# Kernel optimization log

Hardware: AMD Instinct MI355X
Metric: run time of the kernel (lower is better)

## Reference

```python
import jax, jax.numpy as jnp
import numpy as np

N = 100000      # nodes
E = 1600000     # edges
IN_FEATS = 256
HID = 64
N_LAYERS = 3
OUT_FEATS = 32


def _glorot(key, shape):
    lim = np.sqrt(6.0 / (shape[0] + shape[1]))
    return jax.random.uniform(key, shape, jnp.float32, -lim, lim)


def setup_inputs() -> dict:
    key = jax.random.key(0)
    ks = jax.random.split(key, 8)
    feat = jax.random.normal(ks[0], (N, IN_FEATS), jnp.float32)
    src = jax.random.randint(ks[1], (E,), 0, N, jnp.int32)
    dst = jax.random.randint(ks[2], (E,), 0, N, jnp.int32)
    W1 = _glorot(ks[3], (IN_FEATS, HID)); b1 = jnp.zeros((HID,), jnp.float32)
    W2 = _glorot(ks[4], (HID, HID));      b2 = jnp.zeros((HID,), jnp.float32)
    W3 = _glorot(ks[5], (HID, HID));      b3 = jnp.zeros((HID,), jnp.float32)
    Wm = _glorot(ks[6], (HID * N_LAYERS, OUT_FEATS))
    bm = jnp.zeros((OUT_FEATS,), jnp.float32)
    return dict(feat=feat, src=src, dst=dst, W1=W1, b1=b1, W2=W2, b2=b2,
                W3=W3, b3=b3, Wm=Wm, bm=bm)


def _gcn_layer(feat, W, b, src, dst, do_isqrt, di_isqrt):
    # DGL GraphConv, norm='both', eval-mode dropout (identity), ReLU activation.
    # Weight applied before aggregation (mathematically identical, smaller SpMM).
    h = (feat * do_isqrt[:, None]) @ W            # [N, hid]
    agg = jax.ops.segment_sum(h[src], dst, num_segments=N)  # copy_u / sum
    return jax.nn.relu(agg * di_isqrt[:, None] + b)


def reference(feat, src, dst, W1, b1, W2, b2, W3, b3, Wm, bm):
    ones = jnp.ones((E,), jnp.float32)
    deg_out = jnp.clip(jax.ops.segment_sum(ones, src, num_segments=N), 1.0)
    deg_in = jnp.clip(jax.ops.segment_sum(ones, dst, num_segments=N), 1.0)
    do_isqrt = deg_out ** -0.5
    di_isqrt = deg_in ** -0.5

    h1 = _gcn_layer(feat, W1, b1, src, dst, do_isqrt, di_isqrt)
    h2 = _gcn_layer(h1, W2, b2, src, dst, do_isqrt, di_isqrt)
    h3 = _gcn_layer(h2, W3, b3, src, dst, do_isqrt, di_isqrt)

    # Jumping knowledge: mode='cat'
    h = jnp.concatenate([h1, h2, h3], axis=-1)    # [N, 192]
    # Final un-normalized message pass: copy_u / sum
    h = jax.ops.segment_sum(h[src], dst, num_segments=N)
    return h @ Wm + bm                            # [N, 32]
```

## Files before the change

### kernel.cpp

```cpp
#include <hip/hip_runtime.h>
#include <hip/hip_fp8.h>

#define IN_FEATS 256
#define HID 64
#define OUTF 32
#define JK (3*HID)

#define NB    128
#define BSH   10
#define NBLK2 256

typedef __attribute__((ext_vector_type(4))) float floatx4;
typedef __attribute__((ext_vector_type(8))) short shortx8;

__device__ inline unsigned short f2bf(float f) {
    unsigned u = __float_as_uint(f);
    unsigned r = (u + 0x7fffu + ((u >> 16) & 1u)) >> 16;
    return (unsigned short)r;
}
__device__ inline float bf2f(unsigned short u) {
    return __uint_as_float(((unsigned)u) << 16);
}
__device__ inline unsigned pack2(float a, float b) {
    return (unsigned)f2bf(a) | ((unsigned)f2bf(b) << 16);
}
__device__ inline unsigned char f2q(float f) {
    __hip_fp8_e4m3 q(f);
    return (unsigned char)q.__x;
}
__device__ inline float q2f(unsigned char b) {
    union { unsigned char c; __hip_fp8_e4m3 q; } u;
    u.c = b;
    return (float)u.q;
}
__device__ inline void accq8(uint2 u, float* a, float s) {
    a[0] = fmaf(q2f((unsigned char)(u.x      )), s, a[0]);
    a[1] = fmaf(q2f((unsigned char)(u.x >>  8)), s, a[1]);
    a[2] = fmaf(q2f((unsigned char)(u.x >> 16)), s, a[2]);
    a[3] = fmaf(q2f((unsigned char)(u.x >> 24)), s, a[3]);
    a[4] = fmaf(q2f((unsigned char)(u.y      )), s, a[4]);
    a[5] = fmaf(q2f((unsigned char)(u.y >>  8)), s, a[5]);
    a[6] = fmaf(q2f((unsigned char)(u.y >> 16)), s, a[6]);
    a[7] = fmaf(q2f((unsigned char)(u.y >> 24)), s, a[7]);
}
__device__ inline void acc8(uint4 u, float* a) {
    a[0] += bf2f((unsigned short)(u.x & 0xffff)); a[1] += bf2f((unsigned short)(u.x >> 16));
    a[2] += bf2f((unsigned short)(u.y & 0xffff)); a[3] += bf2f((unsigned short)(u.y >> 16));
    a[4] += bf2f((unsigned short)(u.z & 0xffff)); a[5] += bf2f((unsigned short)(u.z >> 16));
    a[6] += bf2f((unsigned short)(u.w & 0xffff)); a[7] += bf2f((unsigned short)(u.w >> 16));
}

__device__ inline void chunk_bounds(int E, int b, int& beg, int& end) {
    int cb = ((E + NBLK2 - 1) / NBLK2 + 3) & ~3;
    beg = b * cb;
    end = min(beg + cb, E);
}

__global__ __launch_bounds__(256) void p1_hist(const int* __restrict__ src,
                                               const int* __restrict__ dst, int E,
                                               int* __restrict__ bhd, int* __restrict__ bhs) {
    __shared__ int hd[NB], hs[NB];
    int b = blockIdx.x;
    for (int t = threadIdx.x; t < NB; t += 256) { hd[t] = 0; hs[t] = 0; }
    __syncthreads();
    int beg, end;
    chunk_bounds(E, b, beg, end);
    int e = beg + threadIdx.x * 4;
    for (; e + 4 <= end; e += 1024) {
        int4 dd = *(const int4*)&dst[e];
        int4 ss = *(const int4*)&src[e];
        atomicAdd(&hd[dd.x >> BSH], 1); atomicAdd(&hd[dd.y >> BSH], 1);
        atomicAdd(&hd[dd.z >> BSH], 1); atomicAdd(&hd[dd.w >> BSH], 1);
        atomicAdd(&hs[ss.x >> BSH], 1); atomicAdd(&hs[ss.y >> BSH], 1);
        atomicAdd(&hs[ss.z >> BSH], 1); atomicAdd(&hs[ss.w >> BSH], 1);
    }
    for (; e < end; ++e) {
        atomicAdd(&hd[dst[e] >> BSH], 1);
        atomicAdd(&hs[src[e] >> BSH], 1);
    }
    __syncthreads();
    for (int t = threadIdx.x; t < NB; t += 256) {
        bhd[b * NB + t] = hd[t];
        bhs[b * NB + t] = hs[t];
    }
}

__global__ __launch_bounds__(256) void p2a_tot(const int* __restrict__ bhd,
                                               const int* __restrict__ bhs,
                                               int* __restrict__ totd, int* __restrict__ tots,
                                               int nblk,
                                               const float* __restrict__ W1, const float* __restrict__ W2,
                                               const float* __restrict__ W3, const float* __restrict__ Wm,
                                               unsigned short* __restrict__ W1t, unsigned short* __restrict__ W2t,
                                               unsigned short* __restrict__ W3t, unsigned short* __restrict__ Wmt) {
    if ((int)blockIdx.x >= 2 * NB) {
        int i = (blockIdx.x - 2 * NB) * 256 + threadIdx.x;
        if (i < 256 * 64) { int k = i / 64, c = i % 64; W1t[c * 256 + k] = f2bf(W1[i]); return; }
        int j = i - 256 * 64;
        if (j < 64 * 64) { int k = j / 64, c = j % 64; W2t[c * 64 + k] = f2bf(W2[j]); return; }
        int j2 = j - 64 * 64;
        if (j2 < 64 * 64) { int k = j2 / 64, c = j2 % 64; W3t[c * 64 + k] = f2bf(W3[j2]); return; }
        int j3 = j2 - 64 * 64;
        if (j3 < 192 * 32) { int k = j3 / 32, c = j3 % 32; Wmt[c * 192 + k] = f2bf(Wm[j3]); }
        return;
    }
    __shared__ int s[256];
    int side = blockIdx.x >> 7;
    int t = blockIdx.x & (NB - 1);
    const int* bh = side ? bhs : bhd;
    int acc = 0;
    for (int k = threadIdx.x; k < nblk; k += 256) acc += bh[k * NB + t];
    s[threadIdx.x] = acc;
    __syncthreads();
    for (int off = 128; off > 0; off >>= 1) {
        if (threadIdx.x < off) s[threadIdx.x] += s[threadIdx.x + off];
        __syncthreads();
    }
    if (threadIdx.x == 0) (side ? tots : totd)[t] = s[0];
}

__global__ __launch_bounds__(128) void p2b_scan(const int* __restrict__ totd,
                                                const int* __restrict__ tots,
                                                int* __restrict__ based, int* __restrict__ bases) {
    __shared__ int s[NB];
    const int* tot = blockIdx.x ? tots : totd;
    int* bb = blockIdx.x ? bases : based;
    int t = threadIdx.x;
    int v = tot[t];
    s[t] = v;
    __syncthreads();
    for (int off = 1; off < NB; off <<= 1) {
        int u = (t >= off) ? s[t - off] : 0;
        __syncthreads();
        s[t] += u;
        __syncthreads();
    }
    bb[t] = s[t] - v;
    if (t == NB - 1) bb[NB] = s[NB - 1];
}

__global__ __launch_bounds__(256) void p2c_off(int* __restrict__ bhd, int* __restrict__ bhs,
                                               const int* __restrict__ based,
                                               const int* __restrict__ bases, int nblk) {
    __shared__ int s[256];
    int side = blockIdx.x >> 7;
    int t = blockIdx.x & (NB - 1);
    int* bh = side ? bhs : bhd;
    int carry = (side ? bases : based)[t];
    for (int k0 = 0; k0 < nblk; k0 += 256) {
        int k = k0 + threadIdx.x;
        int v = (k < nblk) ? bh[k * NB + t] : 0;
        s[threadIdx.x] = v;
        __syncthreads();
        for (int off = 1; off < 256; off <<= 1) {
            int u = (threadIdx.x >= off) ? s[threadIdx.x - off] : 0;
            __syncthreads();
            s[threadIdx.x] += u;
            __syncthreads();
        }
        if (k < nblk) bh[k * NB + t] = carry + s[threadIdx.x] - v;
        int tot = s[255];
        __syncthreads();
        carry += tot;
    }
}

__global__ __launch_bounds__(256) void p3m(
    const int* __restrict__ src, const int* __restrict__ dst, int E,
    const int* __restrict__ bhd, const int* __restrict__ bhs,
    int* __restrict__ pairbuf, int* __restrict__ srctmp,
    const float* __restrict__ feat, const unsigned short* __restrict__ W1t,
    unsigned char* __restrict__ outq, int nrows) {
    __shared__ int curd[NB], curs[NB];
    __shared__ unsigned short Al[64 * 64];
    __shared__ unsigned short Bl[64 * 64];

    if ((int)blockIdx.x < NBLK2) {
        int b = blockIdx.x;
        for (int t = threadIdx.x; t < NB; t += 256) {
            curd[t] = bhd[b * NB + t];
            curs[t] = bhs[b * NB + t];
        }
        __syncthreads();
        int beg, end;
        chunk_bounds(E, b, beg, end);
        int e = beg + threadIdx.x * 4;
        for (; e + 4 <= end; e += 1024) {
            int4 dd = *(const int4*)&dst[e];
            int4 ss = *(const int4*)&src[e];
            int p0 = atomicAdd(&curd[dd.x >> BSH], 1); pairbuf[p0] = ((dd.x & 1023) << 17) | ss.x;
            int p1 = atomicAdd(&curd[dd.y >> BSH], 1); pairbuf[p1] = ((dd.y & 1023) << 17) | ss.y;
            int p2 = atomicAdd(&curd[dd.z >> BSH], 1); pairbuf[p2] = ((dd.z & 1023) << 17) | ss.z;
            int p3 = atomicAdd(&curd[dd.w >> BSH], 1); pairbuf[p3] = ((dd.w & 1023) << 17) | ss.w;
            int q0 = atomicAdd(&curs[ss.x >> BSH], 1); srctmp[q0] = ss.x;
            int q1 = atomicAdd(&curs[ss.y >> BSH], 1); srctmp[q1] = ss.y;
            int q2 = atomicAdd(&curs[ss.z >> BSH], 1); srctmp[q2] = ss.z;
            int q3 = atomicAdd(&curs[ss.w >> BSH], 1); srctmp[q3] = ss.w;
        }
        for (; e < end; ++e) {
            int d = dst[e], sv = src[e];
            int pd = atomicAdd(&curd[d >> BSH], 1);
            pairbuf[pd] = ((d & 1023) << 17) | sv;
            int ps = atomicAdd(&curs[sv >> BSH], 1);
            srctmp[ps] = sv;
        }
        return;
    }
    const int tid = threadIdx.x;
    const int wave = tid >> 6, lane = tid & 63;
    const int g = lane >> 4, lm = lane & 15;
    const int gr0 = (blockIdx.x - NBLK2) * 64;

    floatx4 acc[4];
    #pragma unroll
    for (int f = 0; f < 4; ++f) acc[f] = (floatx4)0.f;

    for (int kc = 0; kc < IN_FEATS; kc += 64) {
        for (int c = tid; c < 64 * 8; c += 256) {
            int row = c >> 3, c8 = c & 7;
            int grow = gr0 + row;
            unsigned short v[8];
            if (grow < nrows) {
                const float* Xf = feat + (size_t)grow * IN_FEATS + kc + c8 * 8;
                #pragma unroll
                for (int j = 0; j < 8; ++j) v[j] = f2bf(Xf[j]);
            } else {
                #pragma unroll
                for (int j = 0; j < 8; ++j) v[j] = 0;
            }
            int off = (row * 64 + c8 * 8) ^ ((row & 7) << 3);
            *(uint4*)&Al[off] = *(uint4*)v;
        }
        for (int c = tid; c < 64 * 8; c += 256) {
            int col = c >> 3, c8 = c & 7;
            uint4 raw = *(const uint4*)&W1t[(size_t)col * IN_FEATS + kc + c8 * 8];
            int off = (col * 64 + c8 * 8) ^ ((col & 7) << 3);
            *(uint4*)&Bl[off] = raw;
        }
        __syncthreads();
        #pragma unroll
        for (int ks = 0; ks < 2; ++ks) {
            int arow = wave * 16 + lm;
            int aoff = (arow * 64 + ks * 32 + g * 8) ^ ((arow & 7) << 3);
            shortx8 afrag = *(shortx8*)&Al[aoff];
            #pragma unroll
            for (int f = 0; f < 4; ++f) {
                int col = f * 16 + lm;
                int boff = (col * 64 + ks * 32 + g * 8) ^ ((col & 7) << 3);
                shortx8 bfrag = *(shortx8*)&Bl[boff];
                acc[f] = __builtin_amdgcn_mfma_f32_16x16x32_bf16(afrag, bfrag, acc[f], 0, 0, 0);
            }
        }
        __syncthreads();
    }
    #pragma unroll
    for (int f = 0; f < 4; ++f) {
        #pragma unroll
        for (int r = 0; r < 4; ++r) {
            int grow = gr0 + wave * 16 + g * 4 + r;
            if (grow < nrows) outq[(size_t)grow * 64 + f * 16 + lm] = f2q(acc[f][r]);
        }
    }
}

__global__ __launch_bounds__(256) void p4c(const int* __restrict__ pairbuf,
                                           const int* __restrict__ srctmp,
                                           const int* __restrict__ based,
                                           const int* __restrict__ bases,
                                           int* __restrict__ indptr, int* __restrict__ colbuf,
                                           float* __restrict__ di_isqrt, float* __restrict__ do_isqrt,
                                           int N, int E, int nbuck) {
    __shared__ int cnt[1024], lp[1024], s[256];
    int t = threadIdx.x;
    if ((int)blockIdx.x >= nbuck) {
        int b = blockIdx.x - nbuck;
        int nbase = b << BSH;
        int nn = min(1024, N - nbase);
        #pragma unroll
        for (int i = 0; i < 4; ++i) cnt[t + 256 * i] = 0;
        __syncthreads();
        int eb = bases[b], ee = bases[b + 1];
        for (int e = eb + t; e < ee; e += 256)
            atomicAdd(&cnt[srctmp[e] - nbase], 1);
        __syncthreads();
        for (int i = t; i < nn; i += 256)
            do_isqrt[nbase + i] = rsqrtf((float)max(cnt[i], 1));
        return;
    }
    int b = blockIdx.x;
    int nbase = b << BSH;
    int nn = min(1024, N - nbase);
    #pragma unroll
    for (int i = 0; i < 4; ++i) cnt[t + 256 * i] = 0;
    __syncthreads();
    int eb = based[b], ee = based[b + 1];
    for (int e = eb + t; e < ee; e += 256)
        atomicAdd(&cnt[pairbuf[e] >> 17], 1);
    __syncthreads();
    int c0 = cnt[4 * t], c1 = cnt[4 * t + 1], c2 = cnt[4 * t + 2], c3 = cnt[4 * t + 3];
    int psum = c0 + c1 + c2 + c3;
    s[t] = psum;
    __syncthreads();
    for (int off = 1; off < 256; off <<= 1) {
        int v = (t >= off) ? s[t - off] : 0;
        __syncthreads();
        s[t] += v;
        __syncthreads();
    }
    int base = s[t] - psum;
    lp[4 * t] = base;
    lp[4 * t + 1] = base + c0;
    lp[4 * t + 2] = base + c0 + c1;
    lp[4 * t + 3] = base + c0 + c1 + c2;
    __syncthreads();
    for (int i = t; i < nn; i += 256) {
        indptr[nbase + i] = eb + lp[i];
        di_isqrt[nbase + i] = rsqrtf((float)max(cnt[i], 1));
    }
    if (b == 0 && t == 0) indptr[N] = E;
    __syncthreads();
    for (int e = eb + t; e < ee; e += 256) {
        int pk = pairbuf[e];
        int pos = atomicAdd(&lp[pk >> 17], 1);
        colbuf[eb + pos] = pk & 0x1FFFF;
    }
}

template <int COLS, int K, bool OFP8>
__global__ __launch_bounds__(256) void mgemm(
    const unsigned short* __restrict__ X, int ldx,
    const unsigned short* __restrict__ Wt,
    const float* __restrict__ rs,
    void* __restrict__ outv, int ldo, int nrows) {
    constexpr int NFRAG = COLS / 16;
    __shared__ unsigned short Al[64 * K];
    __shared__ unsigned short Bl[COLS * K];

    const int tid = threadIdx.x;
    const int wave = tid >> 6, lane = tid & 63;
    const int g = lane >> 4, lm = lane & 15;
    const int gr0 = blockIdx.x * 64;

    for (int c = tid; c < 64 * (K / 8); c += 256) {
        int row = c / (K / 8), c8 = c % (K / 8);
        int grow = gr0 + row;
        unsigned short v[8];
        if (grow < nrows) {
            uint4 raw = *(const uint4*)(X + (size_t)grow * ldx + c8 * 8);
            unsigned short* rp = (unsigned short*)&raw;
            if (rs) {
                float sc = rs[grow];
                #pragma unroll
                for (int j = 0; j < 8; ++j) v[j] = f2bf(bf2f(rp[j]) * sc);
            } else {
                #pragma unroll
                for (int j = 0; j < 8; ++j) v[j] = rp[j];
            }
        } else {
            #pragma unroll
            for (int j = 0; j < 8; ++j) v[j] = 0;
        }
        int off = (row * K + c8 * 8) ^ ((row & 7) << 3);
        *(uint4*)&Al[off] = *(uint4*)v;
    }
    for (int c = tid; c < COLS * (K / 8); c += 256) {
        int col = c / (K / 8), c8 = c % (K / 8);
        uint4 raw = *(const uint4*)&Wt[(size_t)col * K + c8 * 8];
        int off = (col * K + c8 * 8) ^ ((col & 7) << 3);
        *(uint4*)&Bl[off] = raw;
    }
    __syncthreads();

    floatx4 acc[NFRAG];
    #pragma unroll
    for (int f = 0; f < NFRAG; ++f) acc[f] = (floatx4)0.f;
    int arow = wave * 16 + lm;
    #pragma unroll
    for (int ks = 0; ks < K / 32; ++ks) {
        int aoff = (arow * K + ks * 32 + g * 8) ^ ((arow & 7) << 3);
        shortx8 afrag = *(shortx8*)&Al[aoff];
        #pragma unroll
        for (int f = 0; f < NFRAG; ++f) {
            int col = f * 16 + lm;
            int boff = (col * K + ks * 32 + g * 8) ^ ((col & 7) << 3);
            shortx8 bfrag = *(shortx8*)&Bl[boff];
            acc[f] = __builtin_amdgcn_mfma_f32_16x16x32_bf16(afrag, bfrag, acc[f], 0, 0, 0);
        }
    }
    #pragma unroll
    for (int f = 0; f < NFRAG; ++f) {
        #pragma unroll
        for (int r = 0; r < 4; ++r) {
            int grow = gr0 + wave * 16 + g * 4 + r;
            if (grow < nrows) {
                if (OFP8) {
                    ((unsigned char*)outv)[(size_t)grow * ldo + f * 16 + lm] = f2q(acc[f][r]);
                } else {
                    ((unsigned short*)outv)[(size_t)grow * ldo + f * 16 + lm] = f2bf(acc[f][r]);
                }
            }
        }
    }
}

template <bool DOV>
__global__ __launch_bounds__(256) void gatherH(
    const int* __restrict__ indptr, const int* __restrict__ colbuf,
    const uint2* __restrict__ finq,
    const float* __restrict__ dov,
    const float* __restrict__ di, const float* __restrict__ bias,
    uint4* __restrict__ hout, int ldh, int coff, int N) {
    int j = threadIdx.x & 7;
    int node = blockIdx.x * 32 + (threadIdx.x >> 3);
    if (node >= N) return;
    int beg = indptr[node], end = indptr[node + 1];
    float a[8] = {};
    int e = beg;
    for (; e + 4 <= end; e += 4) {
        int4 cc = *(const int4*)&colbuf[e];
        uint2 u0 = finq[(size_t)cc.x * 8 + j];
        uint2 u1 = finq[(size_t)cc.y * 8 + j];
        uint2 u2 = finq[(size_t)cc.z * 8 + j];
        uint2 u3 = finq[(size_t)cc.w * 8 + j];
        accq8(u0, a, DOV ? dov[cc.x] : 1.0f);
        accq8(u1, a, DOV ? dov[cc.y] : 1.0f);
        accq8(u2, a, DOV ? dov[cc.z] : 1.0f);
        accq8(u3, a, DOV ? dov[cc.w] : 1.0f);
    }
    for (; e < end; ++e) {
        int c = colbuf[e];
        accq8(finq[(size_t)c * 8 + j], a, DOV ? dov[c] : 1.0f);
    }
    float dval = di[node];
    float4 b0 = *(const float4*)&bias[j * 8];
    float4 b1 = *(const float4*)&bias[j * 8 + 4];
    float r[8];
    r[0] = fmaxf(a[0] * dval + b0.x, 0.f); r[1] = fmaxf(a[1] * dval + b0.y, 0.f);
    r[2] = fmaxf(a[2] * dval + b0.z, 0.f); r[3] = fmaxf(a[3] * dval + b0.w, 0.f);
    r[4] = fmaxf(a[4] * dval + b1.x, 0.f); r[5] = fmaxf(a[5] * dval + b1.y, 0.f);
    r[6] = fmaxf(a[6] * dval + b1.z, 0.f); r[7] = fmaxf(a[7] * dval + b1.w, 0.f);
    uint4 o;
    o.x = pack2(r[0], r[1]); o.y = pack2(r[2], r[3]);
    o.z = pack2(r[4], r[5]); o.w = pack2(r[6], r[7]);
    hout[(size_t)node * ldh + coff + j] = o;
}

__global__ __launch_bounds__(256) void final_gather(
    const int* __restrict__ indptr, const int* __restrict__ colbuf,
    const uint4* __restrict__ P4,
    const float* __restrict__ bm,
    float* __restrict__ out, int N) {
    int j = threadIdx.x & 3;
    int node = blockIdx.x * 64 + (threadIdx.x >> 2);
    if (node >= N) return;
    int beg = indptr[node], end = indptr[node + 1];
    float a[8] = {};
    int e = beg;
    for (; e + 4 <= end; e += 4) {
        int4 cc = *(const int4*)&colbuf[e];
        uint4 u0 = P4[(size_t)cc.x * 4 + j];
        uint4 u1 = P4[(size_t)cc.y * 4 + j];
        uint4 u2 = P4[(size_t)cc.z * 4 + j];
        uint4 u3 = P4[(size_t)cc.w * 4 + j];
        acc8(u0, a); acc8(u1, a); acc8(u2, a); acc8(u3, a);
    }
    for (; e < end; ++e) acc8(P4[(size_t)colbuf[e] * 4 + j], a);
    float4 b0 = *(const float4*)&bm[j * 8];
    float4 b1 = *(const float4*)&bm[j * 8 + 4];
    float4 o0 = make_float4(a[0] + b0.x, a[1] + b0.y, a[2] + b0.z, a[3] + b0.w);
    float4 o1 = make_float4(a[4] + b1.x, a[5] + b1.y, a[6] + b1.z, a[7] + b1.w);
    *(float4*)&out[(size_t)node * 32 + j * 8] = o0;
    *(float4*)&out[(size_t)node * 32 + j * 8 + 4] = o1;
}

extern "C" void kernel_launch(void* const* d_in, const int* in_sizes, int n_in,
                              void* d_out, int out_size, void* d_ws, size_t ws_size,
                              hipStream_t stream) {
    const float* feat = (const float*)d_in[0];
    const int*   src  = (const int*)d_in[1];
    const int*   dst  = (const int*)d_in[2];
    const float* W1   = (const float*)d_in[3];
    const float* b1   = (const float*)d_in[4];
    const float* W2   = (const float*)d_in[5];
    const float* b2   = (const float*)d_in[6];
    const float* W3   = (const float*)d_in[7];
    const float* b3   = (const float*)d_in[8];
    const float* Wm   = (const float*)d_in[9];
    const float* bm   = (const float*)d_in[10];
    float* out = (float*)d_out;

    const int N = in_sizes[0] / IN_FEATS;
    const int E = in_sizes[1];
    const int NBUCK = (N + 1023) >> BSH;

    char* wsp = (char*)d_ws;
    auto alloc = [&](size_t bytes) {
        void* p = (void*)wsp;
        wsp += ((bytes + 255) / 256) * 256;
        return p;
    };
    int*   indptr   = (int*)alloc((size_t)(N + 1) * 4);
    int*   colbuf   = (int*)alloc((size_t)E * 4);
    int*   bhd      = (int*)alloc((size_t)NBLK2 * NB * 4);
    int*   bhs      = (int*)alloc((size_t)NBLK2 * NB * 4);
    int*   totd     = (int*)alloc(NB * 4);
    int*   tots     = (int*)alloc(NB * 4);
    int*   based    = (int*)alloc((NB + 1) * 4);
    int*   bases    = (int*)alloc((NB + 1) * 4);
    float* do_isqrt = (float*)alloc((size_t)N * 4);
    float* di_isqrt = (float*)alloc((size_t)N * 4);
    unsigned short* W1t = (unsigned short*)alloc(256 * 64 * 2);
    unsigned short* W2t = (unsigned short*)alloc(64 * 64 * 2);
    unsigned short* W3t = (unsigned short*)alloc(64 * 64 * 2);
    unsigned short* Wmt = (unsigned short*)alloc(192 * 32 * 2);
    unsigned short* Hb  = (unsigned short*)alloc((size_t)N * JK * 2);
    int*   pairbuf  = (int*)alloc((size_t)E * 4);
    int*   srctmp   = (int*)alloc((size_t)E * 4);
    unsigned char* tmpq = (unsigned char*)alloc((size_t)N * HID);
    unsigned short* P   = (unsigned short*)alloc((size_t)N * OUTF * 2);

    const int GB = (N + 63) / 64;
    const int GGB = (N + 31) / 32;

    p1_hist<<<NBLK2, 256, 0, stream>>>(src, dst, E, bhd, bhs);
    p2a_tot<<<2 * NB + 120, 256, 0, stream>>>(bhd, bhs, totd, tots, NBLK2,
                                              W1, W2, W3, Wm, W1t, W2t, W3t, Wmt);
    p2b_scan<<<2, NB, 0, stream>>>(totd, tots, based, bases);
    p2c_off<<<2 * NB, 256, 0, stream>>>(bhd, bhs, based, bases, NBLK2);
    p3m<<<NBLK2 + GB, 256, 0, stream>>>(src, dst, E, bhd, bhs, pairbuf, srctmp,
                                        feat, W1t, tmpq, N);
    p4c<<<2 * NBUCK, 256, 0, stream>>>(pairbuf, srctmp, based, bases, indptr, colbuf,
                                       di_isqrt, do_isqrt, N, E, NBUCK);

    gatherH<true><<<GGB, 256, 0, stream>>>(indptr, colbuf, (const uint2*)tmpq, do_isqrt,
                                           di_isqrt, b1, (uint4*)Hb, 24, 0, N);
    mgemm<HID, HID, true><<<GB, 256, 0, stream>>>(Hb, JK, W2t, do_isqrt, tmpq, HID, N);
    gatherH<false><<<GGB, 256, 0, stream>>>(indptr, colbuf, (const uint2*)tmpq, nullptr,
                                            di_isqrt, b2, (uint4*)Hb, 24, 8, N);
    mgemm<HID, HID, true><<<GB, 256, 0, stream>>>(Hb + HID, JK, W3t, do_isqrt, tmpq, HID, N);
    gatherH<false><<<GGB, 256, 0, stream>>>(indptr, colbuf, (const uint2*)tmpq, nullptr,
                                            di_isqrt, b3, (uint4*)Hb, 24, 16, N);
    mgemm<OUTF, JK, false><<<GB, 256, 0, stream>>>(Hb, JK, Wmt, nullptr, P, OUTF, N);
    final_gather<<<(N + 63) / 64, 256, 0, stream>>>(indptr, colbuf, (const uint4*)P, bm, out, N);
}
```

Before: 225.7 us.

## Split dst/src scatter into separate blocks and widen CSR build blocks to 1024 threads

The edge scatter in p3m now runs the dst-pair scatter and the src scatter in separate block groups (2*NBLK2 blocks instead of NBLK2), so each block carries half the work and fewer LDS atomics in flight. The p4c CSR build kernel now uses 1024-thread blocks, one thread per node in the bucket, replacing the per-thread 4-element scan with a 1024-wide Hillis-Steele scan. This raises parallelism in the preprocessing, at the cost of reading src twice and a longer scan with more barriers.

After: 205.4 us. 9.0% less time.

```diff
diff --git a/kernel.cpp b/kernel.cpp
--- a/kernel.cpp
+++ b/kernel.cpp
@@ -171,16 +171,13 @@
     int* __restrict__ pairbuf, int* __restrict__ srctmp,
     const float* __restrict__ feat, const unsigned short* __restrict__ W1t,
     unsigned char* __restrict__ outq, int nrows) {
-    __shared__ int curd[NB], curs[NB];
+    __shared__ int cur[NB];
     __shared__ unsigned short Al[64 * 64];
     __shared__ unsigned short Bl[64 * 64];
 
     if ((int)blockIdx.x < NBLK2) {
         int b = blockIdx.x;
-        for (int t = threadIdx.x; t < NB; t += 256) {
-            curd[t] = bhd[b * NB + t];
-            curs[t] = bhs[b * NB + t];
-        }
+        for (int t = threadIdx.x; t < NB; t += 256) cur[t] = bhd[b * NB + t];
         __syncthreads();
         int beg, end;
         chunk_bounds(E, b, beg, end);
@@ -188,20 +185,35 @@
         for (; e + 4 <= end; e += 1024) {
             int4 dd = *(const int4*)&dst[e];
             int4 ss = *(const int4*)&src[e];
-            int p0 = atomicAdd(&curd[dd.x >> BSH], 1); pairbuf[p0] = ((dd.x & 1023) << 17) | ss.x;
-            int p1 = atomicAdd(&curd[dd.y >> BSH], 1); pairbuf[p1] = ((dd.y & 1023) << 17) | ss.y;
-            int p2 = atomicAdd(&curd[dd.z >> BSH], 1); pairbuf[p2] = ((dd.z & 1023) << 17) | ss.z;
-            int p3 = atomicAdd(&curd[dd.w >> BSH], 1); pairbuf[p3] = ((dd.w & 1023) << 17) | ss.w;
-            int q0 = atomicAdd(&curs[ss.x >> BSH], 1); srctmp[q0] = ss.x;
-            int q1 = atomicAdd(&curs[ss.y >> BSH], 1); srctmp[q1] = ss.y;
-            int q2 = atomicAdd(&curs[ss.z >> BSH], 1); srctmp[q2] = ss.z;
-            int q3 = atomicAdd(&curs[ss.w >> BSH], 1); srctmp[q3] = ss.w;
+            int p0 = atomicAdd(&cur[dd.x >> BSH], 1); pairbuf[p0] = ((dd.x & 1023) << 17) | ss.x;
+            int p1 = atomicAdd(&cur[dd.y >> BSH], 1); pairbuf[p1] = ((dd.y & 1023) << 17) | ss.y;
+            int p2 = atomicAdd(&cur[dd.z >> BSH], 1); pairbuf[p2] = ((dd.z & 1023) << 17) | ss.z;
+            int p3 = atomicAdd(&cur[dd.w >> BSH], 1); pairbuf[p3] = ((dd.w & 1023) << 17) | ss.w;
         }
         for (; e < end; ++e) {
             int d = dst[e], sv = src[e];
-            int pd = atomicAdd(&curd[d >> BSH], 1);
+            int pd = atomicAdd(&cur[d >> BSH], 1);
             pairbuf[pd] = ((d & 1023) << 17) | sv;
-            int ps = atomicAdd(&curs[sv >> BSH], 1);
+        }
+        return;
+    }
+    if ((int)blockIdx.x < 2 * NBLK2) {
+        int b = blockIdx.x - NBLK2;
+        for (int t = threadIdx.x; t < NB; t += 256) cur[t] = bhs[b * NB + t];
+        __syncthreads();
+        int beg, end;
+        chunk_bounds(E, b, beg, end);
+        int e = beg + threadIdx.x * 4;
+        for (; e + 4 <= end; e += 1024) {
+            int4 ss = *(const int4*)&src[e];
+            int q0 = atomicAdd(&cur[ss.x >> BSH], 1); srctmp[q0] = ss.x;
+            int q1 = atomicAdd(&cur[ss.y >> BSH], 1); srctmp[q1] = ss.y;
+            int q2 = atomicAdd(&cur[ss.z >> BSH], 1); srctmp[q2] = ss.z;
+            int q3 = atomicAdd(&cur[ss.w >> BSH], 1); srctmp[q3] = ss.w;
+        }
+        for (; e < end; ++e) {
+            int sv = src[e];
+            int ps = atomicAdd(&cur[sv >> BSH], 1);
             srctmp[ps] = sv;
         }
         return;
@@ -209,7 +221,7 @@
     const int tid = threadIdx.x;
     const int wave = tid >> 6, lane = tid & 63;
     const int g = lane >> 4, lm = lane & 15;
-    const int gr0 = (blockIdx.x - NBLK2) * 64;
+    const int gr0 = (blockIdx.x - 2 * NBLK2) * 64;
 
     floatx4 acc[4];
     #pragma unroll
@@ -263,63 +275,55 @@
     }
 }
 
-__global__ __launch_bounds__(256) void p4c(const int* __restrict__ pairbuf,
-                                           const int* __restrict__ srctmp,
-                                           const int* __restrict__ based,
-                                           const int* __restrict__ bases,
-                                           int* __restrict__ indptr, int* __restrict__ colbuf,
-                                           float* __restrict__ di_isqrt, float* __restrict__ do_isqrt,
-                                           int N, int E, int nbuck) {
-    __shared__ int cnt[1024], lp[1024], s[256];
+__global__ __launch_bounds__(1024) void p4c(const int* __restrict__ pairbuf,
+                                            const int* __restrict__ srctmp,
+                                            const int* __restrict__ based,
+                                            const int* __restrict__ bases,
+                                            int* __restrict__ indptr, int* __restrict__ colbuf,
+                                            float* __restrict__ di_isqrt, float* __restrict__ do_isqrt,
+                                            int N, int E, int nbuck) {
+    __shared__ int cnt[1024], lp[1024], s[1024];
     int t = threadIdx.x;
     if ((int)blockIdx.x >= nbuck) {
         int b = blockIdx.x - nbuck;
         int nbase = b << BSH;
         int nn = min(1024, N - nbase);
-        #pragma unroll
-        for (int i = 0; i < 4; ++i) cnt[t + 256 * i] = 0;
+        cnt[t] = 0;
         __syncthreads();
         int eb = bases[b], ee = bases[b + 1];
-        for (int e = eb + t; e < ee; e += 256)
+        for (int e = eb + t; e < ee; e += 1024)
             atomicAdd(&cnt[srctmp[e] - nbase], 1);
         __syncthreads();
-        for (int i = t; i < nn; i += 256)
-            do_isqrt[nbase + i] = rsqrtf((float)max(cnt[i], 1));
+        if (t < nn) do_isqrt[nbase + t] = rsqrtf((float)max(cnt[t], 1));
         return;
     }
     int b = blockIdx.x;
     int nbase = b << BSH;
     int nn = min(1024, N - nbase);
-    #pragma unroll
-    for (int i = 0; i < 4; ++i) cnt[t + 256 * i] = 0;
+    cnt[t] = 0;
     __syncthreads();
     int eb = based[b], ee = based[b + 1];
-    for (int e = eb + t; e < ee; e += 256)
+    for (int e = eb + t; e < ee; e += 1024)
         atomicAdd(&cnt[pairbuf[e] >> 17], 1);
     __syncthreads();
-    int c0 = cnt[4 * t], c1 = cnt[4 * t + 1], c2 = cnt[4 * t + 2], c3 = cnt[4 * t + 3];
-    int psum = c0 + c1 + c2 + c3;
-    s[t] = psum;
-    __syncthreads();
-    for (int off = 1; off < 256; off <<= 1) {
+    int own = cnt[t];
+    s[t] = own;
+    __syncthreads();
+    for (int off = 1; off < 1024; off <<= 1) {
         int v = (t >= off) ? s[t - off] : 0;
         __syncthreads();
         s[t] += v;
         __syncthreads();
     }
-    int base = s[t] - psum;
-    lp[4 * t] = base;
-    lp[4 * t + 1] = base + c0;
-    lp[4 * t + 2] = base + c0 + c1;
-    lp[4 * t + 3] = base + c0 + c1 + c2;
-    __syncthreads();
-    for (int i = t; i < nn; i += 256) {
-        indptr[nbase + i] = eb + lp[i];
-        di_isqrt[nbase + i] = rsqrtf((float)max(cnt[i], 1));
+    lp[t] = s[t] - own;
+    __syncthreads();
+    if (t < nn) {
+        indptr[nbase + t] = eb + lp[t];
+        di_isqrt[nbase + t] = rsqrtf((float)max(own, 1));
     }
     if (b == 0 && t == 0) indptr[N] = E;
     __syncthreads();
-    for (int e = eb + t; e < ee; e += 256) {
+    for (int e = eb + t; e < ee; e += 1024) {
         int pk = pairbuf[e];
         int pos = atomicAdd(&lp[pk >> 17], 1);
         colbuf[eb + pos] = pk & 0x1FFFF;
@@ -527,10 +531,10 @@
                                               W1, W2, W3, Wm, W1t, W2t, W3t, Wmt);
     p2b_scan<<<2, NB, 0, stream>>>(totd, tots, based, bases);
     p2c_off<<<2 * NB, 256, 0, stream>>>(bhd, bhs, based, bases, NBLK2);
-    p3m<<<NBLK2 + GB, 256, 0, stream>>>(src, dst, E, bhd, bhs, pairbuf, srctmp,
-                                        feat, W1t, tmpq, N);
-    p4c<<<2 * NBUCK, 256, 0, stream>>>(pairbuf, srctmp, based, bases, indptr, colbuf,
-                                       di_isqrt, do_isqrt, N, E, NBUCK);
+    p3m<<<2 * NBLK2 + GB, 256, 0, stream>>>(src, dst, E, bhd, bhs, pairbuf, srctmp,
+                                            feat, W1t, tmpq, N);
+    p4c<<<2 * NBUCK, 1024, 0, stream>>>(pairbuf, srctmp, based, bases, indptr, colbuf,
+                                        di_isqrt, do_isqrt, N, E, NBUCK);
 
     gatherH<true><<<GGB, 256, 0, stream>>>(indptr, colbuf, (const uint2*)tmpq, do_isqrt,
                                            di_isqrt, b1, (uint4*)Hb, 24, 0, N);
```
